# Optimization experiments

Hardware: AMD Instinct MI355X
Metric: run time of the kernel (lower is better)

Reference implementation:

```python
import jax, jax.numpy as jnp
import numpy as np

DEPTH = 9
NUM_LEAVES = 2 ** DEPTH            # 512
NUM_BRANCHES = 2 ** DEPTH - 1      # 511


def _leaf_paths(depth):
    """For each leaf, the BFS (heap-order) branch indices along its root->leaf
    path and the left/right bit taken at each branch (1 = right)."""
    L = 2 ** depth
    idx = np.zeros((L, depth), np.int32)
    bits = np.zeros((L, depth), np.int32)
    for l in range(L):
        node = 0
        for t in range(depth):
            b = (l >> (depth - 1 - t)) & 1
            idx[l, t] = node
            bits[l, t] = b
            node = 2 * node + 1 + b
    return jnp.asarray(idx), jnp.asarray(bits)

PATH_IDX, PATH_BITS = _leaf_paths(DEPTH)


def setup_inputs() -> dict:
    key = jax.random.key(0)
    k1, k2, k3 = jax.random.split(key, 3)
    B, D, W, H = 128, 256, 28, 28
    C = 200
    return {
        "xs": jax.random.normal(k1, (B, D, W, H), jnp.float32),
        "prototypes": jax.random.normal(k2, (NUM_BRANCHES, D, 1, 1), jnp.float32),
        "leaf_params": jax.random.normal(k3, (NUM_LEAVES, C), jnp.float32),
    }


def reference(xs, prototypes, leaf_params):
    # ---- L2Conv2D: squared-L2 distance map via conv decomposition ----
    B, D, W, H = xs.shape
    P = prototypes.shape[0]
    p = prototypes.reshape(P, D)                       # W1 = H1 = 1
    x2 = jnp.sum(xs * xs, axis=1)                      # [B, W, H]
    p2 = jnp.sum(p * p, axis=1)                        # [P]
    xp = jnp.einsum('bdwh,pd->bpwh', xs, p)            # [B, P, W, H]
    sq = x2[:, None] - 2.0 * xp + p2[None, :, None, None]
    distances = jnp.sqrt(jnp.abs(sq) + 1e-14)          # [B, P, W, H]

    # ---- min-pool over full spatial extent (avg-pool unused: focal off) ----
    min_distances = jnp.min(distances, axis=(2, 3))    # [B, P]
    similarities = jnp.exp(-min_distances)             # [B, P], ps per branch

    # ---- soft tree routing: pa(leaf) = prod over path of ps / (1-ps) ----
    ps_path = similarities[:, PATH_IDX]                # [B, L, depth]
    step = jnp.where(PATH_BITS[None] == 1, ps_path, 1.0 - ps_path)
    pa = jnp.prod(step, axis=-1)                       # [B, L]

    # ---- mix leaf class distributions (distributed sampling strategy) ----
    ds = jax.nn.softmax(leaf_params, axis=-1)          # [L, C]
    return pa @ ds                                     # [B, C]
```

## Files before the change

### kernel.cpp

```cpp
#include <hip/hip_runtime.h>
#include <hip/hip_bf16.h>

typedef __attribute__((ext_vector_type(8))) short bf16x8;
typedef __attribute__((ext_vector_type(4))) float f32x4;

#define D_K    256
#define WH     784
#define WHH    392
#define P_REAL 511
#define P_PAD  512
#define C_OUT  200
#define NLEAF  512
#define TDEPTH 9

#define NT      32
#define NTILES  13
#define TILE_USH 8192

#define WS_PB   0
#define WS_P2   262144
#define WS_DS   264192
#define WS_PM   673792

static __device__ __forceinline__ unsigned short f2bf(float x) {
    union { float f; unsigned int u; } v; v.f = x;
    unsigned int r = v.u + 0x7FFFu + ((v.u >> 16) & 1u);
    return (unsigned short)(r >> 16);
}

__global__ __launch_bounds__(64)
void prep2_kernel(const float* __restrict__ protos, const float* __restrict__ lp,
                  unsigned short* __restrict__ pb, float* __restrict__ p2,
                  float* __restrict__ ds) {
    int bid = blockIdx.x;
    int l = threadIdx.x;
    if (bid < P_PAD) {
        int p = bid;
        f32x4 v = {0.f, 0.f, 0.f, 0.f};
        if (p < P_REAL)
            v = *reinterpret_cast<const f32x4*>(protos + (size_t)p * D_K + 4 * l);
        ushort4 w;
        w.x = f2bf(-2.f * v[0]); w.y = f2bf(-2.f * v[1]);
        w.z = f2bf(-2.f * v[2]); w.w = f2bf(-2.f * v[3]);
        *reinterpret_cast<ushort4*>(pb + (size_t)p * D_K + 4 * l) = w;
        float s = v[0]*v[0] + v[1]*v[1] + v[2]*v[2] + v[3]*v[3];
#pragma unroll
        for (int m = 32; m >= 1; m >>= 1) s += __shfl_xor(s, m, 64);
        if (l == 0) p2[p] = s;
    } else {
        int row = bid - P_PAD;
        float v[4];
        float mx = -3.4e38f;
#pragma unroll
        for (int i = 0; i < 4; ++i) {
            int c = l + 64 * i;
            v[i] = (c < C_OUT) ? lp[(size_t)row * C_OUT + c] : -3.4e38f;
            mx = fmaxf(mx, v[i]);
        }
#pragma unroll
        for (int m = 32; m >= 1; m >>= 1) mx = fmaxf(mx, __shfl_xor(mx, m, 64));
        float sum = 0.f;
#pragma unroll
        for (int i = 0; i < 4; ++i) {
            int c = l + 64 * i;
            if (c < C_OUT) { v[i] = expf(v[i] - mx); sum += v[i]; }
        }
#pragma unroll
        for (int m = 32; m >= 1; m >>= 1) sum += __shfl_xor(sum, m, 64);
        float inv = 1.f / sum;
#pragma unroll
        for (int i = 0; i < 4; ++i) {
            int c = l + 64 * i;
            if (c < C_OUT) ds[(size_t)row * C_OUT + c] = v[i] * inv;
        }
    }
}

__global__ __launch_bounds__(512, 2)
void proto_min_kernel(const float* __restrict__ xs,
                      const unsigned short* __restrict__ pb,
                      float* __restrict__ pm) {
    __shared__ unsigned short Xs[2][TILE_USH];
    __shared__ float x2buf[2][8*68 + 8];

    const int tid  = threadIdx.x;
    const int wv   = tid >> 6;
    const int lane = tid & 63;
    const int g    = lane >> 4;
    const int lr   = lane & 15;

    const int b   = blockIdx.x >> 1;
    const int whh = blockIdx.x & 1;

    const float* xb = xs + (size_t)b * (D_K * WH) + whh * WHH;

    bf16x8 af[4][8];
#pragma unroll
    for (int mf = 0; mf < 4; ++mf) {
        const unsigned short* rp = pb + (size_t)(64*wv + 16*mf + lr) * D_K + 8*g;
#pragma unroll
        for (int ks = 0; ks < 8; ++ks)
            af[mf][ks] = *reinterpret_cast<const bf16x8*>(rp + 32*ks);
    }

    const int n4 = tid & 7;
    const int kq = tid >> 3;

    float rmin[4][4];
#pragma unroll
    for (int mf = 0; mf < 4; ++mf)
#pragma unroll
        for (int r = 0; r < 4; ++r) rmin[mf][r] = 3.0e38f;

    f32x4 ld[4];

#define LOAD_TILE(T) do {                                                     \
        int colb = (T) * NT + 4 * n4;                                         \
        if (colb > WHH - 4) colb = WHH - 4;                                   \
        const float* rowp = xb + (size_t)(4*kq) * WH + colb;                  \
        _Pragma("unroll")                                                     \
        for (int r = 0; r < 4; ++r)                                           \
            ld[r] = *reinterpret_cast<const f32x4*>(rowp + r * WH);           \
    } while (0)

#define STAGE_TILE(DST) do {                                                  \
        f32x4 x2a = {0.f, 0.f, 0.f, 0.f};                                     \
        _Pragma("unroll")                                                     \
        for (int r = 0; r < 4; ++r) {                                         \
            f32x4 v = ld[r];                                                  \
            x2a[0] += v[0]*v[0]; x2a[1] += v[1]*v[1];                         \
            x2a[2] += v[2]*v[2]; x2a[3] += v[3]*v[3];                         \
        }                                                                     \
        _Pragma("unroll")                                                     \
        for (int c = 0; c < 4; ++c) {                                         \
            int n = 4*n4 + c;                                                 \
            int key = (n ^ (n >> 2)) & 7;                                     \
            float2 f01 = make_float2(ld[0][c], ld[1][c]);                     \
            float2 f23 = make_float2(ld[2][c], ld[3][c]);                     \
            __hip_bfloat162 b01 = __float22bfloat162_rn(f01);                 \
            __hip_bfloat162 b23 = __float22bfloat162_rn(f23);                 \
            uint2 w;                                                          \
            w.x = *reinterpret_cast<unsigned int*>(&b01);                     \
            w.y = *reinterpret_cast<unsigned int*>(&b23);                     \
            int off = n*256 + (((kq >> 1) ^ key) << 3) + ((kq & 1) << 2);     \
            *reinterpret_cast<uint2*>(&Xs[DST][off]) = w;                     \
        }                                                                     \
        _Pragma("unroll")                                                     \
        for (int c = 0; c < 4; ++c) {                                         \
            x2a[c] += __shfl_xor(x2a[c], 8, 64);                              \
            x2a[c] += __shfl_xor(x2a[c], 16, 64);                             \
            x2a[c] += __shfl_xor(x2a[c], 32, 64);                             \
        }                                                                     \
        if (lane < 8) {                                                       \
            _Pragma("unroll")                                                 \
            for (int c = 0; c < 4; ++c)                                       \
                x2buf[DST][lane*68 + c*8 + wv] = x2a[c];                      \
        }                                                                     \
    } while (0)

    LOAD_TILE(0);
    STAGE_TILE(0);
    __syncthreads();

    int buf = 0;
    for (int t = 0; t < NTILES; ++t) {
        const bool more = (t + 1 < NTILES);

        if (more) LOAD_TILE(t + 1);

        float x2v[2];
#pragma unroll
        for (int nf = 0; nf < 2; ++nf) {
            int n = 16*nf + lr;
            const float* xp = &x2buf[buf][(n >> 2)*68 + (n & 3)*8];
            f32x4 q0 = *reinterpret_cast<const f32x4*>(xp);
            f32x4 q1 = *reinterpret_cast<const f32x4*>(xp + 4);
            x2v[nf] = ((q0[0]+q0[1]) + (q0[2]+q0[3]))
                    + ((q1[0]+q1[1]) + (q1[2]+q1[3]));
        }

        f32x4 acc[4][2];
#pragma unroll
        for (int mf = 0; mf < 4; ++mf) {
            acc[mf][0] = (f32x4){x2v[0], x2v[0], x2v[0], x2v[0]};
            acc[mf][1] = (f32x4){x2v[1], x2v[1], x2v[1], x2v[1]};
        }

        __builtin_amdgcn_s_setprio(1);
#pragma unroll
        for (int ks = 0; ks < 8; ++ks) {
            bf16x8 bfr[2];
#pragma unroll
            for (int nf = 0; nf < 2; ++nf) {
                int n = 16*nf + lr;
                int key = (n ^ (n >> 2)) & 7;
                int off = n*256 + ((((ks << 2) + g) ^ key) << 3);
                bfr[nf] = *reinterpret_cast<const bf16x8*>(&Xs[buf][off]);
            }
#pragma unroll
            for (int mf = 0; mf < 4; ++mf)
#pragma unroll
                for (int nf = 0; nf < 2; ++nf)
                    acc[mf][nf] = __builtin_amdgcn_mfma_f32_16x16x32_bf16(
                        af[mf][ks], bfr[nf], acc[mf][nf], 0, 0, 0);
        }
        __builtin_amdgcn_s_setprio(0);

        if (more) STAGE_TILE(buf ^ 1);

#pragma unroll
        for (int mf = 0; mf < 4; ++mf)
#pragma unroll
            for (int r = 0; r < 4; ++r)
                rmin[mf][r] = fminf(rmin[mf][r],
                                    fminf(acc[mf][0][r], acc[mf][1][r]));

        __syncthreads();
        buf ^= 1;
    }

#pragma unroll
    for (int mf = 0; mf < 4; ++mf)
#pragma unroll
        for (int r = 0; r < 4; ++r) {
            float v = rmin[mf][r];
#pragma unroll
            for (int m = 1; m <= 8; m <<= 1)
                v = fminf(v, __shfl_xor(v, m, 64));
            rmin[mf][r] = v;
        }

    if (lr == 0) {
        float* pmw = pm + ((size_t)b * 2 + whh) * P_PAD;
#pragma unroll
        for (int mf = 0; mf < 4; ++mf)
#pragma unroll
            for (int r = 0; r < 4; ++r)
                pmw[64*wv + 16*mf + 4*g + r] = rmin[mf][r];
    }
#undef LOAD_TILE
#undef STAGE_TILE
}

__global__ __launch_bounds__(256)
void out_kernel(const float* __restrict__ pm, const float* __restrict__ p2,
                const float* __restrict__ ds, float* __restrict__ out) {
    __shared__ float sim[NLEAF];
    __shared__ float pa[NLEAF];
    int b = blockIdx.x;
    int t = threadIdx.x;
    const float* pm0 = pm + (size_t)b * 2 * P_PAD;
#pragma unroll
    for (int j = 0; j < 2; ++j) {
        int p = t + 256 * j;
        float m = fminf(pm0[p], pm0[P_PAD + p]);
        float sq = m + p2[p];
        sim[p] = expf(-sqrtf(fabsf(sq) + 1e-14f));
    }
    __syncthreads();
#pragma unroll
    for (int j = 0; j < 2; ++j) {
        int leaf = t + 256 * j;
        int node = 0;
        float prod = 1.f;
#pragma unroll
        for (int st = 0; st < TDEPTH; ++st) {
            int bit = (leaf >> (TDEPTH - 1 - st)) & 1;
            float sv = sim[node];
            prod *= bit ? sv : (1.f - sv);
            node = 2 * node + 1 + bit;
        }
        pa[leaf] = prod;
    }
    __syncthreads();
    if (t < C_OUT) {
        float a0 = 0.f, a1 = 0.f, a2 = 0.f, a3 = 0.f;
        for (int l = 0; l < NLEAF; l += 4) {
            a0 += pa[l + 0] * ds[(size_t)(l + 0) * C_OUT + t];
            a1 += pa[l + 1] * ds[(size_t)(l + 1) * C_OUT + t];
            a2 += pa[l + 2] * ds[(size_t)(l + 2) * C_OUT + t];
            a3 += pa[l + 3] * ds[(size_t)(l + 3) * C_OUT + t];
        }
        out[(size_t)b * C_OUT + t] = (a0 + a1) + (a2 + a3);
    }
}

extern "C" void kernel_launch(void* const* d_in, const int* in_sizes, int n_in,
                              void* d_out, int out_size, void* d_ws, size_t ws_size,
                              hipStream_t stream) {
    (void)in_sizes; (void)n_in; (void)out_size; (void)ws_size;
    const float* xs     = (const float*)d_in[0];
    const float* protos = (const float*)d_in[1];
    const float* lp     = (const float*)d_in[2];
    float* out = (float*)d_out;

    char* ws = (char*)d_ws;
    unsigned short* pb = (unsigned short*)(ws + WS_PB);
    float* p2   = (float*)(ws + WS_P2);
    float* dsm  = (float*)(ws + WS_DS);
    float* pm   = (float*)(ws + WS_PM);

    prep2_kernel<<<1024, 64, 0, stream>>>(protos, lp, pb, p2, dsm);
    proto_min_kernel<<<256, 512, 0, stream>>>(xs, pb, pm);
    out_kernel<<<128, 256, 0, stream>>>(pm, p2, dsm, out);
}
```

Baseline: 58.05 us.

## Switch prototype-distance GEMM from bf16 MFMA to scaled FP8 MFMA

Prototypes and staged input tiles are now quantized to FP8 (e4m3) with the packed conversion builtin instead of bf16. The inner product uses the 16x16x128 f8f6f4 scaled MFMA with unit scales, so each K pass needs 2 instructions instead of 8. The LDS swizzle, the fragment loads and the workspace layout are adapted to byte-sized elements. This halves the operand bytes and uses the higher-throughput FP8 matrix path, at the cost of much lower precision in the dot products that feed the min-distance.

```diff
diff --git a/kernel.cpp b/kernel.cpp
--- a/kernel.cpp
+++ b/kernel.cpp
@@ -1,7 +1,8 @@
 #include <hip/hip_runtime.h>
 #include <hip/hip_bf16.h>
 
-typedef __attribute__((ext_vector_type(8))) short bf16x8;
+typedef __attribute__((ext_vector_type(8))) int   i32x8;
+typedef __attribute__((ext_vector_type(4))) int   i32x4;
 typedef __attribute__((ext_vector_type(4))) float f32x4;
 
 #define D_K    256
@@ -15,22 +16,18 @@
 
 #define NT      32
 #define NTILES  13
-#define TILE_USH 8192
-
-#define WS_PB   0
-#define WS_P2   262144
-#define WS_DS   264192
-#define WS_PM   673792
-
-static __device__ __forceinline__ unsigned short f2bf(float x) {
-    union { float f; unsigned int u; } v; v.f = x;
-    unsigned int r = v.u + 0x7FFFu + ((v.u >> 16) & 1u);
-    return (unsigned short)(r >> 16);
-}
+#define TILE_B  8192
+
+#define WS_PB8  0
+#define WS_P2   131072
+#define WS_DS   133120
+#define WS_PM   542720
+
+#define SCALE_ONE 0x7F7F7F7F
 
 __global__ __launch_bounds__(64)
 void prep2_kernel(const float* __restrict__ protos, const float* __restrict__ lp,
-                  unsigned short* __restrict__ pb, float* __restrict__ p2,
+                  unsigned char* __restrict__ pb8, float* __restrict__ p2,
                   float* __restrict__ ds) {
     int bid = blockIdx.x;
     int l = threadIdx.x;
@@ -39,10 +36,10 @@
         f32x4 v = {0.f, 0.f, 0.f, 0.f};
         if (p < P_REAL)
             v = *reinterpret_cast<const f32x4*>(protos + (size_t)p * D_K + 4 * l);
-        ushort4 w;
-        w.x = f2bf(-2.f * v[0]); w.y = f2bf(-2.f * v[1]);
-        w.z = f2bf(-2.f * v[2]); w.w = f2bf(-2.f * v[3]);
-        *reinterpret_cast<ushort4*>(pb + (size_t)p * D_K + 4 * l) = w;
+        int u = 0;
+        u = __builtin_amdgcn_cvt_pk_fp8_f32(-2.f * v[0], -2.f * v[1], u, false);
+        u = __builtin_amdgcn_cvt_pk_fp8_f32(-2.f * v[2], -2.f * v[3], u, true);
+        *reinterpret_cast<int*>(pb8 + (size_t)p * D_K + 4 * l) = u;
         float s = v[0]*v[0] + v[1]*v[1] + v[2]*v[2] + v[3]*v[3];
 #pragma unroll
         for (int m = 32; m >= 1; m >>= 1) s += __shfl_xor(s, m, 64);
@@ -78,15 +75,15 @@
 
 __global__ __launch_bounds__(512, 2)
 void proto_min_kernel(const float* __restrict__ xs,
-                      const unsigned short* __restrict__ pb,
+                      const unsigned char* __restrict__ pb8,
                       float* __restrict__ pm) {
-    __shared__ unsigned short Xs[2][TILE_USH];
+    __shared__ unsigned char Xs[2][TILE_B];
     __shared__ float x2buf[2][8*68 + 8];
 
     const int tid  = threadIdx.x;
     const int wv   = tid >> 6;
     const int lane = tid & 63;
-    const int g    = lane >> 4;
+    const int lh   = lane >> 4;
     const int lr   = lane & 15;
 
     const int b   = blockIdx.x >> 1;
@@ -94,23 +91,21 @@
 
     const float* xb = xs + (size_t)b * (D_K * WH) + whh * WHH;
 
-    bf16x8 af[4][8];
+    i32x8 af[4][2];
 #pragma unroll
     for (int mf = 0; mf < 4; ++mf) {
-        const unsigned short* rp = pb + (size_t)(64*wv + 16*mf + lr) * D_K + 8*g;
-#pragma unroll
-        for (int ks = 0; ks < 8; ++ks)
-            af[mf][ks] = *reinterpret_cast<const bf16x8*>(rp + 32*ks);
+        const unsigned char* rp = pb8 + (size_t)(64*wv + 16*mf + lr) * D_K + lh*32;
+        af[mf][0] = *reinterpret_cast<const i32x8*>(rp);
+        af[mf][1] = *reinterpret_cast<const i32x8*>(rp + 128);
     }
 
     const int n4 = tid & 7;
     const int kq = tid >> 3;
 
-    float rmin[4][4];
+    f32x4 rmin[4];
 #pragma unroll
     for (int mf = 0; mf < 4; ++mf)
-#pragma unroll
-        for (int r = 0; r < 4; ++r) rmin[mf][r] = 3.0e38f;
+        rmin[mf] = (f32x4){3.0e38f, 3.0e38f, 3.0e38f, 3.0e38f};
 
     f32x4 ld[4];
 
@@ -135,15 +130,11 @@
         for (int c = 0; c < 4; ++c) {                                         \
             int n = 4*n4 + c;                                                 \
             int key = (n ^ (n >> 2)) & 7;                                     \
-            float2 f01 = make_float2(ld[0][c], ld[1][c]);                     \
-            float2 f23 = make_float2(ld[2][c], ld[3][c]);                     \
-            __hip_bfloat162 b01 = __float22bfloat162_rn(f01);                 \
-            __hip_bfloat162 b23 = __float22bfloat162_rn(f23);                 \
-            uint2 w;                                                          \
-            w.x = *reinterpret_cast<unsigned int*>(&b01);                     \
-            w.y = *reinterpret_cast<unsigned int*>(&b23);                     \
-            int off = n*256 + (((kq >> 1) ^ key) << 3) + ((kq & 1) << 2);     \
-            *reinterpret_cast<uint2*>(&Xs[DST][off]) = w;                     \
+            int u = 0;                                                        \
+            u = __builtin_amdgcn_cvt_pk_fp8_f32(ld[0][c], ld[1][c], u, false);\
+            u = __builtin_amdgcn_cvt_pk_fp8_f32(ld[2][c], ld[3][c], u, true); \
+            int off = n*256 + (((kq >> 2) ^ key) << 4) + ((kq & 3) << 2);     \
+            *reinterpret_cast<int*>(&Xs[DST][off]) = u;                       \
         }                                                                     \
         _Pragma("unroll")                                                     \
         for (int c = 0; c < 4; ++c) {                                         \
@@ -188,21 +179,28 @@
 
         __builtin_amdgcn_s_setprio(1);
 #pragma unroll
-        for (int ks = 0; ks < 8; ++ks) {
-            bf16x8 bfr[2];
+        for (int ks = 0; ks < 2; ++ks) {
+            i32x8 bfr[2];
 #pragma unroll
             for (int nf = 0; nf < 2; ++nf) {
                 int n = 16*nf + lr;
                 int key = (n ^ (n >> 2)) & 7;
-                int off = n*256 + ((((ks << 2) + g) ^ key) << 3);
-                bfr[nf] = *reinterpret_cast<const bf16x8*>(&Xs[buf][off]);
+                int kg0 = ks*8 + lh*2;
+                i32x4 lo = *reinterpret_cast<const i32x4*>(
+                               &Xs[buf][n*256 + ((kg0 ^ key) << 4)]);
+                i32x4 hi = *reinterpret_cast<const i32x4*>(
+                               &Xs[buf][n*256 + (((kg0 + 1) ^ key) << 4)]);
+                bfr[nf] = __builtin_shufflevector(lo, hi, 0,1,2,3,4,5,6,7);
             }
 #pragma unroll
             for (int mf = 0; mf < 4; ++mf)
 #pragma unroll
                 for (int nf = 0; nf < 2; ++nf)
-                    acc[mf][nf] = __builtin_amdgcn_mfma_f32_16x16x32_bf16(
-                        af[mf][ks], bfr[nf], acc[mf][nf], 0, 0, 0);
+                    acc[mf][nf] = __builtin_amdgcn_mfma_scale_f32_16x16x128_f8f6f4(
+                        af[mf][ks], bfr[nf], acc[mf][nf],
+                        0, 0,
+                        0, SCALE_ONE,
+                        0, SCALE_ONE);
         }
         __builtin_amdgcn_s_setprio(0);
 
@@ -236,7 +234,7 @@
         for (int mf = 0; mf < 4; ++mf)
 #pragma unroll
             for (int r = 0; r < 4; ++r)
-                pmw[64*wv + 16*mf + 4*g + r] = rmin[mf][r];
+                pmw[64*wv + 16*mf + 4*lh + r] = rmin[mf][r];
     }
 #undef LOAD_TILE
 #undef STAGE_TILE
@@ -295,12 +293,12 @@
     float* out = (float*)d_out;
 
     char* ws = (char*)d_ws;
-    unsigned short* pb = (unsigned short*)(ws + WS_PB);
+    unsigned char* pb8 = (unsigned char*)(ws + WS_PB8);
     float* p2   = (float*)(ws + WS_P2);
     float* dsm  = (float*)(ws + WS_DS);
     float* pm   = (float*)(ws + WS_PM);
 
-    prep2_kernel<<<1024, 64, 0, stream>>>(protos, lp, pb, p2, dsm);
-    proto_min_kernel<<<256, 512, 0, stream>>>(xs, pb, pm);
+    prep2_kernel<<<1024, 64, 0, stream>>>(protos, lp, pb8, p2, dsm);
+    proto_min_kernel<<<256, 512, 0, stream>>>(xs, pb8, pm);
     out_kernel<<<128, 256, 0, stream>>>(pm, p2, dsm, out);
 }
```

Result: faster. 52.39 us (-9.8%).
